# Performance work log

Measured on AMD Instinct MI355X. Metric: run time of the kernel, lower is better.

The kernel has to match this reference:

```python
import jax, jax.numpy as jnp
import numpy as np

N = 50000          # total nodes across batched graphs
E = 800000         # directed edges (before self-loops)
F_IN = 6           # node_features
HID = 64           # hidden_dim
H = 4              # GAT heads
NG = 1024          # number of graphs in batch
GRID_SIZE = 5      # efficient-kan defaults
SPLINE_K = 3
NEG_SLOPE = 0.2    # GATConv LeakyReLU slope


def setup_inputs() -> dict:
    key = jax.random.key(0)
    ks = jax.random.split(key, 20)
    s = 0.1
    d1 = H * HID  # 256
    inp = {
        "x": jax.random.normal(ks[0], (N, F_IN), dtype=jnp.float32),
        "edge_index": jax.random.randint(ks[1], (2, E), 0, N, dtype=jnp.int64),
        "batch": jnp.sort(jax.random.randint(ks[2], (N,), 0, NG, dtype=jnp.int64)),
        "W1": jax.random.normal(ks[3], (F_IN, d1)) * s,
        "a_src1": jax.random.normal(ks[4], (H, HID)) * s,
        "a_dst1": jax.random.normal(ks[5], (H, HID)) * s,
        "b1": jnp.zeros((d1,), jnp.float32),
        "W2": jax.random.normal(ks[6], (d1, d1)) * s,
        "a_src2": jax.random.normal(ks[7], (H, HID)) * s,
        "a_dst2": jax.random.normal(ks[8], (H, HID)) * s,
        "b2": jnp.zeros((d1,), jnp.float32),
        # KAN layer 1: 256 -> 32
        "base_w1": jax.random.normal(ks[9], (32, d1)) * s,
        "spline_w1": jax.random.normal(ks[10], (32, d1, GRID_SIZE + SPLINE_K)) * s,
        "scaler1": jax.random.normal(ks[11], (32, d1)) * s + 1.0,
        # KAN layer 2: 32 -> 1
        "base_w2": jax.random.normal(ks[12], (1, 32)) * s,
        "spline_w2": jax.random.normal(ks[13], (1, 32, GRID_SIZE + SPLINE_K)) * s,
        "scaler2": jax.random.normal(ks[14], (1, 32)) * s + 1.0,
    }
    return inp


def _gat_conv(x, edge_index, W, a_src, a_dst, bias):
    """PyG GATConv (concat=True, eval mode, self-loops added)."""
    n = x.shape[0]
    src, dst = edge_index[0], edge_index[1]
    xw = (x @ W).reshape(n, H, HID)                      # [N,H,C]
    alpha_s = jnp.einsum('nhc,hc->nh', xw, a_src)        # [N,H]
    alpha_d = jnp.einsum('nhc,hc->nh', xw, a_dst)
    e = alpha_s[src] + alpha_d[dst]                      # [E,H]
    e = jax.nn.leaky_relu(e, NEG_SLOPE)
    # segment softmax over destination nodes
    m = jax.ops.segment_max(e, dst, num_segments=n)      # [N,H]
    ex = jnp.exp(e - m[dst])
    den = jax.ops.segment_sum(ex, dst, num_segments=n)
    alpha = ex / (den[dst] + 1e-16)                      # [E,H]
    msg = alpha[:, :, None] * xw[src]                    # [E,H,C]
    out = jax.ops.segment_sum(msg, dst, num_segments=n)  # [N,H,C]
    return out.reshape(n, H * HID) + bias


def _b_splines(x, grid):
    # x: [B, in]; grid: 1D extended knot vector
    xe = x[..., None]
    b = ((xe >= grid[:-1]) & (xe < grid[1:])).astype(x.dtype)
    for k in range(1, SPLINE_K + 1):
        b = ((xe - grid[:-(k + 1)]) / (grid[k:-1] - grid[:-(k + 1)]) * b[..., :-1]
             + (grid[k + 1:] - xe) / (grid[k + 1:] - grid[1:-k]) * b[..., 1:])
    return b  # [B, in, GRID_SIZE + SPLINE_K]


_H_STEP = 2.0 / GRID_SIZE
_GRID = (jnp.arange(-SPLINE_K, GRID_SIZE + SPLINE_K + 1, dtype=jnp.float32) * _H_STEP - 1.0)


def _kan_linear(x, base_w, spline_w, scaler):
    spline_out = jnp.einsum('nip,oip->no', _b_splines(x, _GRID), spline_w * scaler[..., None])
    return jax.nn.silu(x) @ base_w.T + spline_out


def reference(x, edge_index, batch, W1, a_src1, a_dst1, b1, W2, a_src2, a_dst2, b2,
              base_w1, spline_w1, scaler1, base_w2, spline_w2, scaler2):
    n = x.shape[0]
    loops = jnp.arange(n, dtype=edge_index.dtype)
    ei = jnp.concatenate([edge_index, jnp.stack([loops, loops])], axis=1)  # add self-loops
    h = jax.nn.elu(_gat_conv(x, ei, W1, a_src1, a_dst1, b1))
    h = jax.nn.elu(_gat_conv(h, ei, W2, a_src2, a_dst2, b2))
    # global mean pool over graphs
    sums = jax.ops.segment_sum(h, batch, num_segments=NG)
    cnt = jax.ops.segment_sum(jnp.ones((n,), h.dtype), batch, num_segments=NG)
    pooled = sums / jnp.maximum(cnt, 1.0)[:, None]       # [NG, 256]
    z = _kan_linear(pooled, base_w1, spline_w1, scaler1)  # [NG, 32]
    return _kan_linear(z, base_w2, spline_w2, scaler2)    # [NG, 1]
```

## Files before the change

kernel.cpp:

```cpp
#include <hip/hip_runtime.h>
#include <math.h>

#define HEADS 4
#define HID 64
#define D1 256
#define NGR 1024
#define NEG 0.2f

typedef __attribute__((ext_vector_type(8))) short bf16x8;
typedef __attribute__((ext_vector_type(4))) float f32x4;

static inline int cdiv(int a, int b) { return (a + b - 1) / b; }

__device__ inline unsigned short f2b(float f) {
    union { float f; unsigned u; } v; v.f = f;
    unsigned r = v.u + 0x7FFFu + ((v.u >> 16) & 1u);
    return (unsigned short)(r >> 16);
}
__device__ inline float b2f(unsigned short u) {
    union { unsigned u; float f; } v; v.u = ((unsigned)u) << 16;
    return v.f;
}


__global__ void k_deg(const int* __restrict__ ei, int E, int ET, int* __restrict__ deg) {
    int e = blockIdx.x * blockDim.x + threadIdx.x;
    if (e >= ET) return;
    int d = (e < E) ? ei[E + e] : e - E;
    atomicAdd(&deg[d], 1);
}

__global__ void k_scan1(const int* __restrict__ deg, int* __restrict__ rowp,
                        int* __restrict__ part, int N) {
    __shared__ int sd[256];
    int t = threadIdx.x;
    int i = blockIdx.x * 256 + t;
    int v = (i < N) ? deg[i] : 0;
    sd[t] = v;
    __syncthreads();
    for (int off = 1; off < 256; off <<= 1) {
        int u = (t >= off) ? sd[t - off] : 0;
        __syncthreads();
        sd[t] += u;
        __syncthreads();
    }
    if (i <= N) rowp[i] = sd[t] - v;
    if (t == 255) part[blockIdx.x] = sd[255];
}

__global__ void k_scan2(int* __restrict__ part, int P) {
    __shared__ int sp[1024];
    int t = threadIdx.x;
    int v = (t < P) ? part[t] : 0;
    sp[t] = v;
    __syncthreads();
    for (int off = 1; off < 1024; off <<= 1) {
        int u = (t >= off) ? sp[t - off] : 0;
        __syncthreads();
        sp[t] += u;
        __syncthreads();
    }
    if (t < P) part[t] = sp[t] - v;
}

__global__ void k_scan3(int* __restrict__ rowp, const int* __restrict__ part, int NP1) {
    int i = blockIdx.x * 256 + threadIdx.x;
    if (i < NP1) rowp[i] += part[blockIdx.x];
}

__global__ void k_scatter(const int* __restrict__ ei, int E, int ET,
                          const int* __restrict__ rowp, int* __restrict__ fill,
                          int* __restrict__ csrc) {
    int e = blockIdx.x * blockDim.x + threadIdx.x;
    if (e >= ET) return;
    int s, d;
    if (e < E) { s = ei[e]; d = ei[E + e]; } else { s = d = e - E; }
    int pos = rowp[d] + atomicAdd(&fill[d], 1);
    csrc[pos] = s;
}

__global__ void k_prep(const float* __restrict__ W1, const float* __restrict__ asrc1,
                       const float* __restrict__ adst1, float* __restrict__ va1) {
    int id = threadIdx.x;
    if (id >= 48) return;
    int k = id / 8, h8 = id % 8;
    int h = h8 & 3;
    const float* avec = (h8 < 4) ? (asrc1 + h * HID) : (adst1 + h * HID);
    const float* wrow = W1 + k * D1 + h * HID;
    float s = 0.f;
#pragma unroll 8
    for (int j = 0; j < HID; ++j) s += wrow[j] * avec[j];
    va1[k * 8 + h8] = s;
}

__global__ void k_cvtW(const float* __restrict__ W, const float* __restrict__ asrc2,
                       const float* __restrict__ adst2, unsigned short* __restrict__ Bt) {
    int c = blockIdx.x, k = threadIdx.x;
    float v;
    if (c < 256) {
        v = W[k * D1 + c];
    } else if (c < 264) {
        int h = (c - 256) & 3;
        const float* avec = (c < 260) ? (asrc2 + h * HID) : (adst2 + h * HID);
        const float* wrow = W + k * D1 + h * HID;
        float s = 0.f;
#pragma unroll 8
        for (int j = 0; j < HID; ++j) s += wrow[j] * avec[j];
        v = s;
    } else {
        v = 0.f;
    }
    Bt[c * D1 + k] = f2b(v);
}

__global__ void k_alpha1(const float* __restrict__ x, const float* __restrict__ va1,
                         float* __restrict__ as_, float* __restrict__ ad_, int N) {
    int n = blockIdx.x * blockDim.x + threadIdx.x;
    if (n >= N) return;
    float2 x01 = *(const float2*)(x + n * 6);
    float2 x23 = *(const float2*)(x + n * 6 + 2);
    float2 x45 = *(const float2*)(x + n * 6 + 4);
    float xv[6] = {x01.x, x01.y, x23.x, x23.y, x45.x, x45.y};
    float4 sv, dv;
#pragma unroll
    for (int h = 0; h < 4; ++h) {
        float s = 0.f, d = 0.f;
#pragma unroll
        for (int k = 0; k < 6; ++k) {
            s += xv[k] * va1[k * 8 + h];
            d += xv[k] * va1[k * 8 + 4 + h];
        }
        (&sv.x)[h] = s; (&dv.x)[h] = d;
    }
    ((float4*)as_)[n] = sv;
    ((float4*)ad_)[n] = dv;
}

__global__ void k_aggr1(const int* __restrict__ rowp, const int* __restrict__ csrc,
                        const float* __restrict__ as_, const float* __restrict__ ad_,
                        const float* __restrict__ x, const float* __restrict__ W1,
                        const float* __restrict__ b1, unsigned short* __restrict__ outb, int N) {
    int d = blockIdx.x * 16 + (threadIdx.x >> 4);
    if (d >= N) return;
    int q = threadIdx.x & 15;
    int lo = rowp[d], hi = rowp[d + 1];
    float4 adv = ((const float4*)ad_)[d];

    float a[4][6];
#pragma unroll
    for (int h = 0; h < 4; ++h)
#pragma unroll
        for (int k = 0; k < 6; ++k) a[h][k] = 0.f;
    float den0 = 0.f, den1 = 0.f, den2 = 0.f, den3 = 0.f;
    for (int k = lo + q; k < hi; k += 16) {
        int s = csrc[k];
        float4 av = ((const float4*)as_)[s];
        float l0 = av.x + adv.x; l0 = l0 > 0.f ? l0 : NEG * l0;
        float l1 = av.y + adv.y; l1 = l1 > 0.f ? l1 : NEG * l1;
        float l2 = av.z + adv.z; l2 = l2 > 0.f ? l2 : NEG * l2;
        float l3 = av.w + adv.w; l3 = l3 > 0.f ? l3 : NEG * l3;
        float e0 = __expf(l0);
        float e1 = __expf(l1);
        float e2 = __expf(l2);
        float e3 = __expf(l3);
        den0 += e0; den1 += e1; den2 += e2; den3 += e3;
        float2 x01 = *(const float2*)(x + s * 6);
        float2 x23 = *(const float2*)(x + s * 6 + 2);
        float2 x45 = *(const float2*)(x + s * 6 + 4);
        float xv[6] = {x01.x, x01.y, x23.x, x23.y, x45.x, x45.y};
#pragma unroll
        for (int kk = 0; kk < 6; ++kk) {
            a[0][kk] += e0 * xv[kk];
            a[1][kk] += e1 * xv[kk];
            a[2][kk] += e2 * xv[kk];
            a[3][kk] += e3 * xv[kk];
        }
    }
#pragma unroll
    for (int off = 1; off < 16; off <<= 1) {
        den0 += __shfl_xor(den0, off);
        den1 += __shfl_xor(den1, off);
        den2 += __shfl_xor(den2, off);
        den3 += __shfl_xor(den3, off);
#pragma unroll
        for (int h = 0; h < 4; ++h)
#pragma unroll
            for (int k = 0; k < 6; ++k) a[h][k] += __shfl_xor(a[h][k], off);
    }

    int h = q >> 2;
    float dh = (h == 0) ? den0 : (h == 1) ? den1 : (h == 2) ? den2 : den3;
    float inv = 1.f / (dh + 1e-16f);
    float m[6];
#pragma unroll
    for (int k = 0; k < 6; ++k)
        m[k] = (h == 0) ? a[0][k] : (h == 1) ? a[1][k] : (h == 2) ? a[2][k] : a[3][k];
    int c0 = q * 16;
    unsigned short ob[16];
#pragma unroll
    for (int cc = 0; cc < 16; ++cc) {
        int c = c0 + cc;
        float o = m[0] * W1[c] + m[1] * W1[D1 + c] + m[2] * W1[2 * D1 + c] +
                  m[3] * W1[3 * D1 + c] + m[4] * W1[4 * D1 + c] + m[5] * W1[5 * D1 + c];
        o = o * inv + b1[c];
        o = o > 0.f ? o : (__expf(o) - 1.f);
        ob[cc] = f2b(o);
    }
#pragma unroll
    for (int v = 0; v < 4; ++v)
        ((ushort4*)(outb + (size_t)d * D1 + c0))[v] =
            make_ushort4(ob[v * 4], ob[v * 4 + 1], ob[v * 4 + 2], ob[v * 4 + 3]);
}

__global__ void k_mm(const unsigned short* __restrict__ A, const unsigned short* __restrict__ Bt,
                     unsigned short* __restrict__ C, float* __restrict__ as_,
                     float* __restrict__ ad_, int N) {
    int w = threadIdx.x >> 6;
    int l = threadIdx.x & 63;
    int r0 = blockIdx.x * 64 + w * 16;
    bool half0 = (blockIdx.y == 0);
    int cy = half0 ? 0 : 128;
    int lr = l & 15;
    int lk = (l >> 4) * 8;
    int arow = r0 + lr; if (arow >= N) arow = N - 1;
    const unsigned short* ap = A + (size_t)arow * D1 + lk;
    f32x4 acc[8];
    f32x4 accE = (f32x4){0.f, 0.f, 0.f, 0.f};
#pragma unroll
    for (int i = 0; i < 8; ++i) acc[i] = (f32x4){0.f, 0.f, 0.f, 0.f};
    for (int ks = 0; ks < 8; ++ks) {
        bf16x8 av = *(const bf16x8*)(ap + ks * 32);
#pragma unroll
        for (int ct = 0; ct < 8; ++ct) {
            bf16x8 bv = *(const bf16x8*)(Bt + (size_t)(cy + ct * 16 + lr) * D1 + ks * 32 + lk);
            acc[ct] = __builtin_amdgcn_mfma_f32_16x16x32_bf16(av, bv, acc[ct], 0, 0, 0);
        }
        if (half0) {
            bf16x8 bv = *(const bf16x8*)(Bt + (size_t)(256 + lr) * D1 + ks * 32 + lk);
            accE = __builtin_amdgcn_mfma_f32_16x16x32_bf16(av, bv, accE, 0, 0, 0);
        }
    }
    int rbase = r0 + (l >> 4) * 4;
#pragma unroll
    for (int ct = 0; ct < 8; ++ct) {
#pragma unroll
        for (int r = 0; r < 4; ++r) {
            int row = rbase + r;
            if (row < N) C[(size_t)row * D1 + cy + ct * 16 + lr] = f2b(acc[ct][r]);
        }
    }
    if (half0) {
#pragma unroll
        for (int r = 0; r < 4; ++r) {
            int row = rbase + r;
            if (row < N) {
                float v = accE[r];
                if (lr < 4) as_[row * HEADS + lr] = v;
                else if (lr < 8) ad_[row * HEADS + (lr - 4)] = v;
            }
        }
    }
}

__global__ void k_aggr2(const int* __restrict__ rowp, const int* __restrict__ csrc,
                        const float* __restrict__ as_, const float* __restrict__ ad_,
                        const unsigned short* __restrict__ xb, const float* __restrict__ bias,
                        unsigned short* __restrict__ outb, int N) {
    int d = blockIdx.x * 4 + (threadIdx.x >> 6);
    if (d >= N) return;
    int t = threadIdx.x & 63;
    int h = t >> 4;
    int lo = rowp[d], hi = rowp[d + 1];
    float adh = ad_[d * HEADS + h];

    float4 acc = {0.f, 0.f, 0.f, 0.f};
    float den = 0.f;
    int k = lo;
    for (; k + 3 < hi; k += 4) {
        int s0 = csrc[k], s1 = csrc[k + 1], s2 = csrc[k + 2], s3 = csrc[k + 3];
        float v0 = as_[s0 * HEADS + h] + adh; v0 = v0 > 0.f ? v0 : NEG * v0;
        float v1 = as_[s1 * HEADS + h] + adh; v1 = v1 > 0.f ? v1 : NEG * v1;
        float v2 = as_[s2 * HEADS + h] + adh; v2 = v2 > 0.f ? v2 : NEG * v2;
        float v3 = as_[s3 * HEADS + h] + adh; v3 = v3 > 0.f ? v3 : NEG * v3;
        float e0 = __expf(v0), e1 = __expf(v1);
        float e2 = __expf(v2), e3 = __expf(v3);
        ushort4 u0 = ((const ushort4*)(xb + (size_t)s0 * D1))[t];
        ushort4 u1 = ((const ushort4*)(xb + (size_t)s1 * D1))[t];
        ushort4 u2 = ((const ushort4*)(xb + (size_t)s2 * D1))[t];
        ushort4 u3 = ((const ushort4*)(xb + (size_t)s3 * D1))[t];
        den += e0 + e1 + e2 + e3;
        acc.x += e0 * b2f(u0.x) + e1 * b2f(u1.x) + e2 * b2f(u2.x) + e3 * b2f(u3.x);
        acc.y += e0 * b2f(u0.y) + e1 * b2f(u1.y) + e2 * b2f(u2.y) + e3 * b2f(u3.y);
        acc.z += e0 * b2f(u0.z) + e1 * b2f(u1.z) + e2 * b2f(u2.z) + e3 * b2f(u3.z);
        acc.w += e0 * b2f(u0.w) + e1 * b2f(u1.w) + e2 * b2f(u2.w) + e3 * b2f(u3.w);
    }
    for (; k < hi; ++k) {
        int s0 = csrc[k];
        float v0 = as_[s0 * HEADS + h] + adh; v0 = v0 > 0.f ? v0 : NEG * v0;
        float e0 = __expf(v0);
        ushort4 u0 = ((const ushort4*)(xb + (size_t)s0 * D1))[t];
        den += e0;
        acc.x += e0 * b2f(u0.x); acc.y += e0 * b2f(u0.y);
        acc.z += e0 * b2f(u0.z); acc.w += e0 * b2f(u0.w);
    }
    float inv = 1.f / (den + 1e-16f);
    float4 bv = ((const float4*)bias)[t];
    float4 o;
    o.x = acc.x * inv + bv.x;
    o.y = acc.y * inv + bv.y;
    o.z = acc.z * inv + bv.z;
    o.w = acc.w * inv + bv.w;
    o.x = o.x > 0.f ? o.x : (__expf(o.x) - 1.f);
    o.y = o.y > 0.f ? o.y : (__expf(o.y) - 1.f);
    o.z = o.z > 0.f ? o.z : (__expf(o.z) - 1.f);
    o.w = o.w > 0.f ? o.w : (__expf(o.w) - 1.f);
    ushort4 ub; ub.x = f2b(o.x); ub.y = f2b(o.y); ub.z = f2b(o.z); ub.w = f2b(o.w);
    ((ushort4*)(outb + (size_t)d * D1))[t] = ub;
}


__device__ inline float knotf(int j) { return (j - 3) * 0.4f - 1.0f; }

__device__ inline void bspl8(float x, float* out) {
    float t[12];
#pragma unroll
    for (int j = 0; j < 12; ++j) t[j] = knotf(j);
    float bb[11];
#pragma unroll
    for (int j = 0; j < 11; ++j) bb[j] = (x >= t[j] && x < t[j + 1]) ? 1.f : 0.f;
#pragma unroll
    for (int k = 1; k <= 3; ++k) {
#pragma unroll
        for (int j = 0; j + k < 11; ++j) {
            float dl = t[j + k] - t[j];
            float dr = t[j + k + 1] - t[j + 1];
            bb[j] = (x - t[j]) / dl * bb[j] + (t[j + k + 1] - x) / dr * bb[j + 1];
        }
    }
#pragma unroll
    for (int p = 0; p < 8; ++p) out[p] = bb[p];
}

__device__ inline float siluf(float x) { return x / (1.f + __expf(-x)); }

__global__ void k_poolkan(const unsigned short* __restrict__ hb2, const int* __restrict__ batch,
                          const float* __restrict__ bw1, const float* __restrict__ sw1,
                          const float* __restrict__ sc1, const float* __restrict__ bw2,
                          const float* __restrict__ sw2, const float* __restrict__ sc2,
                          float* __restrict__ out, int N) {
    __shared__ float sB[D1][9];
    __shared__ float sS[D1];
    __shared__ float sZ[32];
    int g = blockIdx.x;
    int lo = 0, hi = N;
    while (lo < hi) { int m = (lo + hi) >> 1; if (batch[m] < g) lo = m + 1; else hi = m; }
    int lo2 = lo, hi2 = N;
    while (lo2 < hi2) { int m = (lo2 + hi2) >> 1; if (batch[m] < g + 1) lo2 = m + 1; else hi2 = m; }
    int i = threadIdx.x;
    float s = 0.f;
    for (int n = lo; n < lo2; ++n) s += b2f(hb2[(size_t)n * D1 + i]);
    float xi = s / (float)max(lo2 - lo, 1);
    float b[8];
    bspl8(xi, b);
#pragma unroll
    for (int p = 0; p < 8; ++p) sB[i][p] = b[p];
    sS[i] = siluf(xi);
    __syncthreads();
    int wv = i >> 6, l = i & 63;
    for (int oo = 0; oo < 8; ++oo) {
        int o = wv * 8 + oo;
        float part = 0.f;
        for (int ii = l; ii < D1; ii += 64) {
            float sc = sc1[o * D1 + ii];
            float p0 = sS[ii] * bw1[o * D1 + ii];
            const float* sw = sw1 + ((size_t)o * D1 + ii) * 8;
#pragma unroll
            for (int p = 0; p < 8; ++p) p0 += sB[ii][p] * sw[p] * sc;
            part += p0;
        }
#pragma unroll
        for (int off = 32; off >= 1; off >>= 1) part += __shfl_down(part, off);
        if (l == 0) sZ[o] = part;
    }
    __syncthreads();
    if (i < 64) {
        float part = 0.f;
        if (i < 32) {
            float z = sZ[i];
            float b2a[8];
            bspl8(z, b2a);
            part = siluf(z) * bw2[i];
            float sc = sc2[i];
#pragma unroll
            for (int p = 0; p < 8; ++p) part += b2a[p] * sw2[i * 8 + p] * sc;
        }
#pragma unroll
        for (int off = 32; off >= 1; off >>= 1) part += __shfl_down(part, off);
        if (i == 0) out[g] = part;
    }
}

extern "C" void kernel_launch(void* const* d_in, const int* in_sizes, int n_in,
                              void* d_out, int out_size, void* d_ws, size_t ws_size,
                              hipStream_t stream) {
    const float* x      = (const float*)d_in[0];
    const int*   ei     = (const int*)d_in[1];
    const int*   batch  = (const int*)d_in[2];
    const float* W1     = (const float*)d_in[3];
    const float* asrc1  = (const float*)d_in[4];
    const float* adst1  = (const float*)d_in[5];
    const float* b1     = (const float*)d_in[6];
    const float* W2     = (const float*)d_in[7];
    const float* asrc2  = (const float*)d_in[8];
    const float* adst2  = (const float*)d_in[9];
    const float* b2     = (const float*)d_in[10];
    const float* bw1    = (const float*)d_in[11];
    const float* sw1    = (const float*)d_in[12];
    const float* sc1    = (const float*)d_in[13];
    const float* bw2    = (const float*)d_in[14];
    const float* sw2    = (const float*)d_in[15];
    const float* sc2    = (const float*)d_in[16];
    float* outp = (float*)d_out;

    const int N  = in_sizes[0] / 6;
    const int E  = in_sizes[1] / 2;
    const int ET = E + N;

    char* base = (char*)d_ws;
    unsigned short* hb  = (unsigned short*)base; base += (size_t)N * D1 * 2;
    unsigned short* xb  = (unsigned short*)base; base += (size_t)N * D1 * 2;
    unsigned short* hb2 = (unsigned short*)base; base += (size_t)N * D1 * 2;
    float* as_ = (float*)base;                   base += (size_t)N * HEADS * 4;
    float* ad_ = (float*)base;                   base += (size_t)N * HEADS * 4;
    unsigned short* Btb = (unsigned short*)base; base += (size_t)272 * D1 * 2;
    float* va1 = (float*)base;                   base += 48 * 4;
    int* deg  = (int*)base;                      base += (size_t)N * 4;
    int* fill = (int*)base;                      base += (size_t)N * 4;
    int* rowp = (int*)base;                      base += (size_t)(N + 1) * 4;
    int* part = (int*)base;                      base += 1024 * 4;
    int* csrc = (int*)base;                      base += (size_t)ET * 4;

    const int TB = 256;
    int gET = cdiv(ET, TB);
    int gSC = cdiv(N + 1, 256);

    hipMemsetAsync(deg, 0, (size_t)N * sizeof(int), stream);
    hipMemsetAsync(fill, 0, (size_t)N * sizeof(int), stream);
    k_prep<<<1, 64, 0, stream>>>(W1, asrc1, adst1, va1);
    k_deg<<<gET, TB, 0, stream>>>(ei, E, ET, deg);
    k_scan1<<<gSC, 256, 0, stream>>>(deg, rowp, part, N);
    k_scan2<<<1, 1024, 0, stream>>>(part, gSC);
    k_scan3<<<gSC, 256, 0, stream>>>(rowp, part, N + 1);
    k_scatter<<<gET, TB, 0, stream>>>(ei, E, ET, rowp, fill, csrc);
    k_cvtW<<<272, 256, 0, stream>>>(W2, asrc2, adst2, Btb);

    k_alpha1<<<cdiv(N, TB), TB, 0, stream>>>(x, va1, as_, ad_, N);
    k_aggr1<<<cdiv(N, 16), TB, 0, stream>>>(rowp, csrc, as_, ad_, x, W1, b1, hb, N);

    k_mm<<<dim3(cdiv(N, 64), 2), TB, 0, stream>>>(hb, Btb, xb, as_, ad_, N);
    k_aggr2<<<cdiv(N, 4), TB, 0, stream>>>(rowp, csrc, as_, ad_, xb, b2, hb2, N);

    k_poolkan<<<NGR, TB, 0, stream>>>(hb2, batch, bw1, sw1, sc1, bw2, sw2, sc2, outp, N);
}
```

Baseline: 307.6 us.

## Precompute normalized per-edge attention weights in a separate kernel for both GAT layers

Adds a k_ew kernel that computes exp(leaky_relu) edge scores per destination, reduces the softmax denominator, and writes normalized per-edge weights to a new buffer. Both aggregation kernels then read these weights instead of recomputing exponentials and denominators. In aggr1 this removes the 4x6 register accumulator and its large shuffle reduction; in aggr2 it removes 64 lanes redundantly recomputing exponentials. The cost is two extra launches and writing and re-reading an E×4 float buffer, about 13 MB per layer.

```diff
diff --git a/kernel.cpp b/kernel.cpp
--- a/kernel.cpp
+++ b/kernel.cpp
@@ -136,73 +136,75 @@
     ((float4*)ad_)[n] = dv;
 }
 
-__global__ void k_aggr1(const int* __restrict__ rowp, const int* __restrict__ csrc,
-                        const float* __restrict__ as_, const float* __restrict__ ad_,
-                        const float* __restrict__ x, const float* __restrict__ W1,
-                        const float* __restrict__ b1, unsigned short* __restrict__ outb, int N) {
+__global__ void k_ew(const int* __restrict__ rowp, const int* __restrict__ csrc,
+                     const float* __restrict__ as_, const float* __restrict__ ad_,
+                     float* __restrict__ wbuf, int N) {
     int d = blockIdx.x * 16 + (threadIdx.x >> 4);
     if (d >= N) return;
     int q = threadIdx.x & 15;
     int lo = rowp[d], hi = rowp[d + 1];
     float4 adv = ((const float4*)ad_)[d];
-
-    float a[4][6];
-#pragma unroll
-    for (int h = 0; h < 4; ++h)
-#pragma unroll
-        for (int k = 0; k < 6; ++k) a[h][k] = 0.f;
-    float den0 = 0.f, den1 = 0.f, den2 = 0.f, den3 = 0.f;
+    float d0 = 0.f, d1 = 0.f, d2 = 0.f, d3 = 0.f;
     for (int k = lo + q; k < hi; k += 16) {
         int s = csrc[k];
         float4 av = ((const float4*)as_)[s];
-        float l0 = av.x + adv.x; l0 = l0 > 0.f ? l0 : NEG * l0;
-        float l1 = av.y + adv.y; l1 = l1 > 0.f ? l1 : NEG * l1;
-        float l2 = av.z + adv.z; l2 = l2 > 0.f ? l2 : NEG * l2;
-        float l3 = av.w + adv.w; l3 = l3 > 0.f ? l3 : NEG * l3;
-        float e0 = __expf(l0);
-        float e1 = __expf(l1);
-        float e2 = __expf(l2);
-        float e3 = __expf(l3);
-        den0 += e0; den1 += e1; den2 += e2; den3 += e3;
+        float e0 = av.x + adv.x; e0 = e0 > 0.f ? e0 : NEG * e0; e0 = __expf(e0);
+        float e1 = av.y + adv.y; e1 = e1 > 0.f ? e1 : NEG * e1; e1 = __expf(e1);
+        float e2 = av.z + adv.z; e2 = e2 > 0.f ? e2 : NEG * e2; e2 = __expf(e2);
+        float e3 = av.w + adv.w; e3 = e3 > 0.f ? e3 : NEG * e3; e3 = __expf(e3);
+        ((float4*)wbuf)[k] = make_float4(e0, e1, e2, e3);
+        d0 += e0; d1 += e1; d2 += e2; d3 += e3;
+    }
+#pragma unroll
+    for (int off = 1; off < 16; off <<= 1) {
+        d0 += __shfl_xor(d0, off);
+        d1 += __shfl_xor(d1, off);
+        d2 += __shfl_xor(d2, off);
+        d3 += __shfl_xor(d3, off);
+    }
+    float i0 = 1.f / (d0 + 1e-16f), i1 = 1.f / (d1 + 1e-16f);
+    float i2 = 1.f / (d2 + 1e-16f), i3 = 1.f / (d3 + 1e-16f);
+    for (int k = lo + q; k < hi; k += 16) {
+        float4 wv = ((const float4*)wbuf)[k];
+        wv.x *= i0; wv.y *= i1; wv.z *= i2; wv.w *= i3;
+        ((float4*)wbuf)[k] = wv;
+    }
+}
+
+__global__ void k_aggr1(const int* __restrict__ rowp, const int* __restrict__ csrc,
+                        const float* __restrict__ wbuf, const float* __restrict__ x,
+                        const float* __restrict__ W1, const float* __restrict__ b1,
+                        unsigned short* __restrict__ outb, int N) {
+    int d = blockIdx.x * 16 + (threadIdx.x >> 4);
+    if (d >= N) return;
+    int q = threadIdx.x & 15;
+    int h = q >> 2, j = q & 3;
+    int lo = rowp[d], hi = rowp[d + 1];
+    float a0 = 0.f, a1 = 0.f, a2 = 0.f, a3 = 0.f, a4 = 0.f, a5 = 0.f;
+    for (int k = lo + j; k < hi; k += 4) {
+        int s = csrc[k];
+        float w = wbuf[k * 4 + h];
         float2 x01 = *(const float2*)(x + s * 6);
         float2 x23 = *(const float2*)(x + s * 6 + 2);
         float2 x45 = *(const float2*)(x + s * 6 + 4);
-        float xv[6] = {x01.x, x01.y, x23.x, x23.y, x45.x, x45.y};
-#pragma unroll
-        for (int kk = 0; kk < 6; ++kk) {
-            a[0][kk] += e0 * xv[kk];
-            a[1][kk] += e1 * xv[kk];
-            a[2][kk] += e2 * xv[kk];
-            a[3][kk] += e3 * xv[kk];
-        }
-    }
-#pragma unroll
-    for (int off = 1; off < 16; off <<= 1) {
-        den0 += __shfl_xor(den0, off);
-        den1 += __shfl_xor(den1, off);
-        den2 += __shfl_xor(den2, off);
-        den3 += __shfl_xor(den3, off);
-#pragma unroll
-        for (int h = 0; h < 4; ++h)
-#pragma unroll
-            for (int k = 0; k < 6; ++k) a[h][k] += __shfl_xor(a[h][k], off);
-    }
-
-    int h = q >> 2;
-    float dh = (h == 0) ? den0 : (h == 1) ? den1 : (h == 2) ? den2 : den3;
-    float inv = 1.f / (dh + 1e-16f);
-    float m[6];
-#pragma unroll
-    for (int k = 0; k < 6; ++k)
-        m[k] = (h == 0) ? a[0][k] : (h == 1) ? a[1][k] : (h == 2) ? a[2][k] : a[3][k];
+        a0 += w * x01.x; a1 += w * x01.y;
+        a2 += w * x23.x; a3 += w * x23.y;
+        a4 += w * x45.x; a5 += w * x45.y;
+    }
+#pragma unroll
+    for (int off = 1; off < 4; off <<= 1) {
+        a0 += __shfl_xor(a0, off); a1 += __shfl_xor(a1, off);
+        a2 += __shfl_xor(a2, off); a3 += __shfl_xor(a3, off);
+        a4 += __shfl_xor(a4, off); a5 += __shfl_xor(a5, off);
+    }
     int c0 = q * 16;
     unsigned short ob[16];
 #pragma unroll
     for (int cc = 0; cc < 16; ++cc) {
         int c = c0 + cc;
-        float o = m[0] * W1[c] + m[1] * W1[D1 + c] + m[2] * W1[2 * D1 + c] +
-                  m[3] * W1[3 * D1 + c] + m[4] * W1[4 * D1 + c] + m[5] * W1[5 * D1 + c];
-        o = o * inv + b1[c];
+        float o = a0 * W1[c] + a1 * W1[D1 + c] + a2 * W1[2 * D1 + c] +
+                  a3 * W1[3 * D1 + c] + a4 * W1[4 * D1 + c] + a5 * W1[5 * D1 + c];
+        o += b1[c];
         o = o > 0.f ? o : (__expf(o) - 1.f);
         ob[cc] = f2b(o);
     }
@@ -263,53 +265,44 @@
 }
 
 __global__ void k_aggr2(const int* __restrict__ rowp, const int* __restrict__ csrc,
-                        const float* __restrict__ as_, const float* __restrict__ ad_,
-                        const unsigned short* __restrict__ xb, const float* __restrict__ bias,
-                        unsigned short* __restrict__ outb, int N) {
+                        const float* __restrict__ wbuf, const unsigned short* __restrict__ xb,
+                        const float* __restrict__ bias, unsigned short* __restrict__ outb, int N) {
     int d = blockIdx.x * 4 + (threadIdx.x >> 6);
     if (d >= N) return;
     int t = threadIdx.x & 63;
     int h = t >> 4;
     int lo = rowp[d], hi = rowp[d + 1];
-    float adh = ad_[d * HEADS + h];
 
     float4 acc = {0.f, 0.f, 0.f, 0.f};
-    float den = 0.f;
     int k = lo;
     for (; k + 3 < hi; k += 4) {
         int s0 = csrc[k], s1 = csrc[k + 1], s2 = csrc[k + 2], s3 = csrc[k + 3];
-        float v0 = as_[s0 * HEADS + h] + adh; v0 = v0 > 0.f ? v0 : NEG * v0;
-        float v1 = as_[s1 * HEADS + h] + adh; v1 = v1 > 0.f ? v1 : NEG * v1;
-        float v2 = as_[s2 * HEADS + h] + adh; v2 = v2 > 0.f ? v2 : NEG * v2;
-        float v3 = as_[s3 * HEADS + h] + adh; v3 = v3 > 0.f ? v3 : NEG * v3;
-        float e0 = __expf(v0), e1 = __expf(v1);
-        float e2 = __expf(v2), e3 = __expf(v3);
+        float w0 = wbuf[k * 4 + h];
+        float w1 = wbuf[(k + 1) * 4 + h];
+        float w2 = wbuf[(k + 2) * 4 + h];
+        float w3 = wbuf[(k + 3) * 4 + h];
         ushort4 u0 = ((const ushort4*)(xb + (size_t)s0 * D1))[t];
         ushort4 u1 = ((const ushort4*)(xb + (size_t)s1 * D1))[t];
         ushort4 u2 = ((const ushort4*)(xb + (size_t)s2 * D1))[t];
         ushort4 u3 = ((const ushort4*)(xb + (size_t)s3 * D1))[t];
-        den += e0 + e1 + e2 + e3;
-        acc.x += e0 * b2f(u0.x) + e1 * b2f(u1.x) + e2 * b2f(u2.x) + e3 * b2f(u3.x);
-        acc.y += e0 * b2f(u0.y) + e1 * b2f(u1.y) + e2 * b2f(u2.y) + e3 * b2f(u3.y);
-        acc.z += e0 * b2f(u0.z) + e1 * b2f(u1.z) + e2 * b2f(u2.z) + e3 * b2f(u3.z);
-        acc.w += e0 * b2f(u0.w) + e1 * b2f(u1.w) + e2 * b2f(u2.w) + e3 * b2f(u3.w);
+        acc.x += w0 * b2f(u0.x) + w1 * b2f(u1.x) + w2 * b2f(u2.x) + w3 * b2f(u3.x);
+        acc.y += w0 * b2f(u0.y) + w1 * b2f(u1.y) + w2 * b2f(u2.y) + w3 * b2f(u3.y);
+        acc.z += w0 * b2f(u0.z) + w1 * b2f(u1.z) + w2 * b2f(u2.z) + w3 * b2f(u3.z);
+        acc.w += w0 * b2f(u0.w) + w1 * b2f(u1.w) + w2 * b2f(u2.w) + w3 * b2f(u3.w);
     }
     for (; k < hi; ++k) {
         int s0 = csrc[k];
-        float v0 = as_[s0 * HEADS + h] + adh; v0 = v0 > 0.f ? v0 : NEG * v0;
-        float e0 = __expf(v0);
+        float w0 = wbuf[k * 4 + h];
         ushort4 u0 = ((const ushort4*)(xb + (size_t)s0 * D1))[t];
-        den += e0;
-        acc.x += e0 * b2f(u0.x); acc.y += e0 * b2f(u0.y);
-        acc.z += e0 * b2f(u0.z); acc.w += e0 * b2f(u0.w);
-    }
-    float inv = 1.f / (den + 1e-16f);
+        acc.x += w0 * b2f(u0.x); acc.y += w0 * b2f(u0.y);
+        acc.z += w0 * b2f(u0.z); acc.w += w0 * b2f(u0.w);
+    }
     float4 bv = ((const float4*)bias)[t];
     float4 o;
-    o.x = acc.x * inv + bv.x;
-    o.y = acc.y * inv + bv.y;
-    o.z = acc.z * inv + bv.z;
-    o.w = acc.w * inv + bv.w;
+    o.x = acc.x + bv.x;
+    o.y = acc.y + bv.y;
+    o.z = acc.z + bv.z;
+    o.w = acc.w + bv.w;
     o.x = o.x > 0.f ? o.x : (__expf(o.x) - 1.f);
     o.y = o.y > 0.f ? o.y : (__expf(o.y) - 1.f);
     o.z = o.z > 0.f ? o.z : (__expf(o.z) - 1.f);
@@ -439,10 +432,12 @@
     int* rowp = (int*)base;                      base += (size_t)(N + 1) * 4;
     int* part = (int*)base;                      base += 1024 * 4;
     int* csrc = (int*)base;                      base += (size_t)ET * 4;
+    float* wbuf = (float*)base;                  base += (size_t)ET * HEADS * 4;
 
     const int TB = 256;
     int gET = cdiv(ET, TB);
     int gSC = cdiv(N + 1, 256);
+    int g16 = cdiv(N, 16);
 
     hipMemsetAsync(deg, 0, (size_t)N * sizeof(int), stream);
     hipMemsetAsync(fill, 0, (size_t)N * sizeof(int), stream);
@@ -455,10 +450,12 @@
     k_cvtW<<<272, 256, 0, stream>>>(W2, asrc2, adst2, Btb);
 
     k_alpha1<<<cdiv(N, TB), TB, 0, stream>>>(x, va1, as_, ad_, N);
-    k_aggr1<<<cdiv(N, 16), TB, 0, stream>>>(rowp, csrc, as_, ad_, x, W1, b1, hb, N);
+    k_ew<<<g16, TB, 0, stream>>>(rowp, csrc, as_, ad_, wbuf, N);
+    k_aggr1<<<g16, TB, 0, stream>>>(rowp, csrc, wbuf, x, W1, b1, hb, N);
 
     k_mm<<<dim3(cdiv(N, 64), 2), TB, 0, stream>>>(hb, Btb, xb, as_, ad_, N);
-    k_aggr2<<<cdiv(N, 4), TB, 0, stream>>>(rowp, csrc, as_, ad_, xb, b2, hb2, N);
+    k_ew<<<g16, TB, 0, stream>>>(rowp, csrc, as_, ad_, wbuf, N);
+    k_aggr2<<<cdiv(N, 4), TB, 0, stream>>>(rowp, csrc, wbuf, xb, b2, hb2, N);
 
     k_poolkan<<<NGR, TB, 0, stream>>>(hb2, batch, bw1, sw1, sc1, bw2, sw2, sc2, outp, N);
 }
```

Result: slower. 333.1 us (+8.3%).

## Retile GEMM with LDS-staged weights and XCD-aware mapping; per-head aggr1 lanes

Applied to the files above, without the earlier changes.

The second-layer GEMM now stages a 64-column slice of the transposed weights (plus the 8 attention-projection rows) in LDS. Each block covers 256 rows by 64 columns, with each wave holding a 4x4 tile of MFMA accumulators, and block ids are remapped so adjacent tiles land on the same XCD. The first aggregation kernel now assigns 4 lanes per head instead of 16 lanes each holding all heads. That cuts the shuffle reduction from 28 values to 7 and reduces register pressure. The padded weight rows 264-271 are dropped. The trade-offs are more LDS use per block and less parallelism per destination node in aggr1 on high-degree nodes.

```diff
diff --git a/kernel.cpp b/kernel.cpp
--- a/kernel.cpp
+++ b/kernel.cpp
@@ -99,7 +99,7 @@
     float v;
     if (c < 256) {
         v = W[k * D1 + c];
-    } else if (c < 264) {
+    } else {
         int h = (c - 256) & 3;
         const float* avec = (c < 260) ? (asrc2 + h * HID) : (adst2 + h * HID);
         const float* wrow = W + k * D1 + h * HID;
@@ -107,8 +107,6 @@
 #pragma unroll 8
         for (int j = 0; j < HID; ++j) s += wrow[j] * avec[j];
         v = s;
-    } else {
-        v = 0.f;
     }
     Bt[c * D1 + k] = f2b(v);
 }
@@ -143,65 +141,39 @@
     int d = blockIdx.x * 16 + (threadIdx.x >> 4);
     if (d >= N) return;
     int q = threadIdx.x & 15;
+    int h = q >> 2, j = q & 3;
     int lo = rowp[d], hi = rowp[d + 1];
-    float4 adv = ((const float4*)ad_)[d];
-
-    float a[4][6];
-#pragma unroll
-    for (int h = 0; h < 4; ++h)
-#pragma unroll
-        for (int k = 0; k < 6; ++k) a[h][k] = 0.f;
-    float den0 = 0.f, den1 = 0.f, den2 = 0.f, den3 = 0.f;
-    for (int k = lo + q; k < hi; k += 16) {
+    float adh = ad_[d * HEADS + h];
+    float a0 = 0.f, a1 = 0.f, a2 = 0.f, a3 = 0.f, a4 = 0.f, a5 = 0.f;
+    float den = 0.f;
+    for (int k = lo + j; k < hi; k += 4) {
         int s = csrc[k];
-        float4 av = ((const float4*)as_)[s];
-        float l0 = av.x + adv.x; l0 = l0 > 0.f ? l0 : NEG * l0;
-        float l1 = av.y + adv.y; l1 = l1 > 0.f ? l1 : NEG * l1;
-        float l2 = av.z + adv.z; l2 = l2 > 0.f ? l2 : NEG * l2;
-        float l3 = av.w + adv.w; l3 = l3 > 0.f ? l3 : NEG * l3;
-        float e0 = __expf(l0);
-        float e1 = __expf(l1);
-        float e2 = __expf(l2);
-        float e3 = __expf(l3);
-        den0 += e0; den1 += e1; den2 += e2; den3 += e3;
+        float v = as_[s * HEADS + h] + adh;
+        v = v > 0.f ? v : NEG * v;
+        float e = __expf(v);
+        den += e;
         float2 x01 = *(const float2*)(x + s * 6);
         float2 x23 = *(const float2*)(x + s * 6 + 2);
         float2 x45 = *(const float2*)(x + s * 6 + 4);
-        float xv[6] = {x01.x, x01.y, x23.x, x23.y, x45.x, x45.y};
-#pragma unroll
-        for (int kk = 0; kk < 6; ++kk) {
-            a[0][kk] += e0 * xv[kk];
-            a[1][kk] += e1 * xv[kk];
-            a[2][kk] += e2 * xv[kk];
-            a[3][kk] += e3 * xv[kk];
-        }
-    }
-#pragma unroll
-    for (int off = 1; off < 16; off <<= 1) {
-        den0 += __shfl_xor(den0, off);
-        den1 += __shfl_xor(den1, off);
-        den2 += __shfl_xor(den2, off);
-        den3 += __shfl_xor(den3, off);
-#pragma unroll
-        for (int h = 0; h < 4; ++h)
-#pragma unroll
-            for (int k = 0; k < 6; ++k) a[h][k] += __shfl_xor(a[h][k], off);
-    }
-
-    int h = q >> 2;
-    float dh = (h == 0) ? den0 : (h == 1) ? den1 : (h == 2) ? den2 : den3;
-    float inv = 1.f / (dh + 1e-16f);
-    float m[6];
-#pragma unroll
-    for (int k = 0; k < 6; ++k)
-        m[k] = (h == 0) ? a[0][k] : (h == 1) ? a[1][k] : (h == 2) ? a[2][k] : a[3][k];
+        a0 += e * x01.x; a1 += e * x01.y;
+        a2 += e * x23.x; a3 += e * x23.y;
+        a4 += e * x45.x; a5 += e * x45.y;
+    }
+#pragma unroll
+    for (int off = 1; off < 4; off <<= 1) {
+        den += __shfl_xor(den, off);
+        a0 += __shfl_xor(a0, off); a1 += __shfl_xor(a1, off);
+        a2 += __shfl_xor(a2, off); a3 += __shfl_xor(a3, off);
+        a4 += __shfl_xor(a4, off); a5 += __shfl_xor(a5, off);
+    }
+    float inv = 1.f / (den + 1e-16f);
     int c0 = q * 16;
     unsigned short ob[16];
 #pragma unroll
     for (int cc = 0; cc < 16; ++cc) {
         int c = c0 + cc;
-        float o = m[0] * W1[c] + m[1] * W1[D1 + c] + m[2] * W1[2 * D1 + c] +
-                  m[3] * W1[3 * D1 + c] + m[4] * W1[4 * D1 + c] + m[5] * W1[5 * D1 + c];
+        float o = a0 * W1[c] + a1 * W1[D1 + c] + a2 * W1[2 * D1 + c] +
+                  a3 * W1[3 * D1 + c] + a4 * W1[4 * D1 + c] + a5 * W1[5 * D1 + c];
         o = o * inv + b1[c];
         o = o > 0.f ? o : (__expf(o) - 1.f);
         ob[cc] = f2b(o);
@@ -212,51 +184,93 @@
             make_ushort4(ob[v * 4], ob[v * 4 + 1], ob[v * 4 + 2], ob[v * 4 + 3]);
 }
 
+#define BPITCH 264
 __global__ void k_mm(const unsigned short* __restrict__ A, const unsigned short* __restrict__ Bt,
                      unsigned short* __restrict__ C, float* __restrict__ as_,
                      float* __restrict__ ad_, int N) {
-    int w = threadIdx.x >> 6;
-    int l = threadIdx.x & 63;
-    int r0 = blockIdx.x * 64 + w * 16;
-    bool half0 = (blockIdx.y == 0);
-    int cy = half0 ? 0 : 128;
-    int lr = l & 15;
-    int lk = (l >> 4) * 8;
-    int arow = r0 + lr; if (arow >= N) arow = N - 1;
-    const unsigned short* ap = A + (size_t)arow * D1 + lk;
-    f32x4 acc[8];
-    f32x4 accE = (f32x4){0.f, 0.f, 0.f, 0.f};
-#pragma unroll
-    for (int i = 0; i < 8; ++i) acc[i] = (f32x4){0.f, 0.f, 0.f, 0.f};
+    __shared__ unsigned short sb[80 * BPITCH];
+    int nwg = gridDim.x;
+    int bid = blockIdx.x;
+    int xcd = bid & 7, off = bid >> 3;
+    int qq = nwg >> 3, rr = nwg & 7;
+    int lin = (xcd < rr) ? (xcd * (qq + 1) + off) : (rr * (qq + 1) + (xcd - rr) * qq + off);
+    int xblk = lin >> 2, y = lin & 3;
+
+    int t = threadIdx.x;
+#pragma unroll
+    for (int c = 0; c < 10; ++c) {
+        int idx = c * 256 + t;
+        int r = idx >> 5, ch = idx & 31;
+        uint4 v = make_uint4(0, 0, 0, 0);
+        int src = -1;
+        if (r < 64) src = y * 64 + r;
+        else if (r < 72 && y == 0) src = 256 + (r - 64);
+        if (src >= 0) v = *(const uint4*)(Bt + (size_t)src * D1 + ch * 8);
+        *(uint4*)(&sb[r * BPITCH + ch * 8]) = v;
+    }
+    __syncthreads();
+
+    int w = t >> 6, l = t & 63;
+    int lr = l & 15, lk = (l >> 4) * 8;
+    int r0w = xblk * 256 + w * 64;
+    const unsigned short* aptr[4];
+#pragma unroll
+    for (int m = 0; m < 4; ++m) {
+        int ar = r0w + m * 16 + lr;
+        if (ar >= N) ar = N - 1;
+        aptr[m] = A + (size_t)ar * D1 + lk;
+    }
+    f32x4 acc[4][4];
+    f32x4 accE[4];
+#pragma unroll
+    for (int m = 0; m < 4; ++m) {
+        accE[m] = (f32x4){0.f, 0.f, 0.f, 0.f};
+#pragma unroll
+        for (int n = 0; n < 4; ++n) acc[m][n] = (f32x4){0.f, 0.f, 0.f, 0.f};
+    }
+#pragma unroll
     for (int ks = 0; ks < 8; ++ks) {
-        bf16x8 av = *(const bf16x8*)(ap + ks * 32);
-#pragma unroll
-        for (int ct = 0; ct < 8; ++ct) {
-            bf16x8 bv = *(const bf16x8*)(Bt + (size_t)(cy + ct * 16 + lr) * D1 + ks * 32 + lk);
-            acc[ct] = __builtin_amdgcn_mfma_f32_16x16x32_bf16(av, bv, acc[ct], 0, 0, 0);
-        }
-        if (half0) {
-            bf16x8 bv = *(const bf16x8*)(Bt + (size_t)(256 + lr) * D1 + ks * 32 + lk);
-            accE = __builtin_amdgcn_mfma_f32_16x16x32_bf16(av, bv, accE, 0, 0, 0);
-        }
-    }
-    int rbase = r0 + (l >> 4) * 4;
-#pragma unroll
-    for (int ct = 0; ct < 8; ++ct) {
+        bf16x8 av[4];
+#pragma unroll
+        for (int m = 0; m < 4; ++m) av[m] = *(const bf16x8*)(aptr[m] + ks * 32);
+#pragma unroll
+        for (int n = 0; n < 4; ++n) {
+            bf16x8 bv = *(const bf16x8*)(&sb[(n * 16 + lr) * BPITCH + ks * 32 + lk]);
+#pragma unroll
+            for (int m = 0; m < 4; ++m)
+                acc[m][n] = __builtin_amdgcn_mfma_f32_16x16x32_bf16(av[m], bv, acc[m][n], 0, 0, 0);
+        }
+        if (y == 0) {
+            bf16x8 be = *(const bf16x8*)(&sb[(64 + lr) * BPITCH + ks * 32 + lk]);
+#pragma unroll
+            for (int m = 0; m < 4; ++m)
+                accE[m] = __builtin_amdgcn_mfma_f32_16x16x32_bf16(av[m], be, accE[m], 0, 0, 0);
+        }
+    }
+    int rsub = (l >> 4) * 4;
+#pragma unroll
+    for (int m = 0; m < 4; ++m) {
 #pragma unroll
         for (int r = 0; r < 4; ++r) {
-            int row = rbase + r;
-            if (row < N) C[(size_t)row * D1 + cy + ct * 16 + lr] = f2b(acc[ct][r]);
-        }
-    }
-    if (half0) {
-#pragma unroll
-        for (int r = 0; r < 4; ++r) {
-            int row = rbase + r;
+            int row = r0w + m * 16 + rsub + r;
             if (row < N) {
-                float v = accE[r];
-                if (lr < 4) as_[row * HEADS + lr] = v;
-                else if (lr < 8) ad_[row * HEADS + (lr - 4)] = v;
+#pragma unroll
+                for (int n = 0; n < 4; ++n)
+                    C[(size_t)row * D1 + y * 64 + n * 16 + lr] = f2b(acc[m][n][r]);
+            }
+        }
+    }
+    if (y == 0) {
+#pragma unroll
+        for (int m = 0; m < 4; ++m) {
+#pragma unroll
+            for (int r = 0; r < 4; ++r) {
+                int row = r0w + m * 16 + rsub + r;
+                if (row < N) {
+                    float v = accE[m][r];
+                    if (lr < 4) as_[row * HEADS + lr] = v;
+                    else if (lr < 8) ad_[row * HEADS + (lr - 4)] = v;
+                }
             }
         }
     }
@@ -432,7 +446,7 @@
     unsigned short* hb2 = (unsigned short*)base; base += (size_t)N * D1 * 2;
     float* as_ = (float*)base;                   base += (size_t)N * HEADS * 4;
     float* ad_ = (float*)base;                   base += (size_t)N * HEADS * 4;
-    unsigned short* Btb = (unsigned short*)base; base += (size_t)272 * D1 * 2;
+    unsigned short* Btb = (unsigned short*)base; base += (size_t)264 * D1 * 2;
     float* va1 = (float*)base;                   base += 48 * 4;
     int* deg  = (int*)base;                      base += (size_t)N * 4;
     int* fill = (int*)base;                      base += (size_t)N * 4;
@@ -452,12 +466,12 @@
     k_scan2<<<1, 1024, 0, stream>>>(part, gSC);
     k_scan3<<<gSC, 256, 0, stream>>>(rowp, part, N + 1);
     k_scatter<<<gET, TB, 0, stream>>>(ei, E, ET, rowp, fill, csrc);
-    k_cvtW<<<272, 256, 0, stream>>>(W2, asrc2, adst2, Btb);
+    k_cvtW<<<264, 256, 0, stream>>>(W2, asrc2, adst2, Btb);
 
     k_alpha1<<<cdiv(N, TB), TB, 0, stream>>>(x, va1, as_, ad_, N);
     k_aggr1<<<cdiv(N, 16), TB, 0, stream>>>(rowp, csrc, as_, ad_, x, W1, b1, hb, N);
 
-    k_mm<<<dim3(cdiv(N, 64), 2), TB, 0, stream>>>(hb, Btb, xb, as_, ad_, N);
+    k_mm<<<cdiv(N, 256) * 4, TB, 0, stream>>>(hb, Btb, xb, as_, ad_, N);
     k_aggr2<<<cdiv(N, 4), TB, 0, stream>>>(rowp, csrc, as_, ad_, xb, b2, hb2, N);
 
     k_poolkan<<<NGR, TB, 0, stream>>>(hb2, batch, bw1, sw1, sc1, bw2, sw2, sc2, outp, N);
```

New measurement: 286.2 us. 7.0% less time.
